# Kernel optimization log

Hardware: AMD Instinct MI355X
Metric: run time of the kernel (lower is better)

The kernel has to match this reference:

```python
import jax, jax.numpy as jnp
from jax import lax
import numpy as np

D_X, D_Y, HID = 64, 1, 128
D_NODES = D_X + 2          # d_x + 2
D_IN = D_X + 1 + D_Y       # fc_in input dim
K_LANGEVIN, ETA = 20, 0.01
BATCH = 8192


def setup_inputs() -> dict:
    key = jax.random.key(0)
    ks = jax.random.split(key, 12)
    s = 0.05
    return {
        "x": jax.random.normal(ks[0], (BATCH, D_X), jnp.float32),
        "t": jnp.ones((BATCH, 1), jnp.float32),
        "B_param": s * jax.random.normal(ks[1], (D_NODES, D_NODES), jnp.float32),
        "W_in": s * jax.random.normal(ks[2], (D_IN, HID), jnp.float32),
        "b_in": jnp.zeros((HID,), jnp.float32),
        "WT1": s * jax.random.normal(ks[3], (HID, HID), jnp.float32),
        "bT1": jnp.zeros((HID,), jnp.float32),
        "WT2": s * jax.random.normal(ks[4], (HID, 1), jnp.float32),
        "bT2": jnp.zeros((1,), jnp.float32),
        "WY1": s * jax.random.normal(ks[5], (HID, HID), jnp.float32),
        "bY1": jnp.zeros((HID,), jnp.float32),
        "WY2": s * jax.random.normal(ks[6], (HID, 1), jnp.float32),
        "bY2": jnp.zeros((1,), jnp.float32),
    }


def _mask():
    m = jnp.ones((D_NODES, D_NODES), jnp.float32)
    m = m.at[-1, :D_X].set(0.0)          # last node has no incoming edges from x-nodes
    m = m * (1.0 - jnp.eye(D_NODES, dtype=jnp.float32))  # zero diagonal
    return m


def _energy(z, x, B_param, mask, W_in, b_in, WT1, bT1, WT2, bT2, WY1, bY1, WY2, bY2):
    # z = [t, y] : [B, 1 + d_y]
    A = jax.nn.sigmoid(B_param) * mask                       # [N, N]
    h0 = jnp.concatenate([x, z], axis=-1) @ W_in + b_in      # [B, H]
    h = jnp.broadcast_to(h0[:, None, :], (h0.shape[0], D_NODES, HID))  # repeat over nodes
    # MaskedGraphConv: h + (A @ h) / d_nodes, then ReLU (x2)
    h = jax.nn.relu(h + jnp.einsum('ij,bjd->bid', A, h) / D_NODES)
    h = jax.nn.relu(h + jnp.einsum('ij,bjd->bid', A, h) / D_NODES)
    eT = jax.nn.relu(h[:, -2] @ WT1 + bT1) @ WT2 + bT2       # [B, 1]
    eY = jax.nn.relu(h[:, -1] @ WY1 + bY1) @ WY2 + bY2       # [B, 1]
    return (eT + eY)[:, 0]                                   # [B]


def reference(x, t, B_param, W_in, b_in, WT1, bT1, WT2, bT2, WY1, bY1, WY2, bY2):
    mask = _mask()
    grad_E = jax.grad(lambda z: _energy(z, x, B_param, mask, W_in, b_in,
                                        WT1, bT1, WT2, bT2, WY1, bY1, WY2, bY2).sum())
    z0 = jnp.concatenate([t, jnp.zeros((x.shape[0], D_Y), x.dtype)], axis=-1)
    sqrt_eta = jnp.sqrt(jnp.float32(ETA))

    def step(z, k):
        g = grad_E(z)
        noise = jax.random.normal(k, z.shape, z.dtype)
        return z - 0.5 * ETA * g + sqrt_eta * noise, None

    keys = jax.random.split(jax.random.key(42), K_LANGEVIN)
    z_final, _ = lax.scan(step, z0, keys)
    return z_final[:, 1:]   # predicted y, [B, d_y]
```

## Files before the change

### kernel.cpp

```cpp
#include <hip/hip_runtime.h>
#include <stdint.h>

#define NBATCH 8192
#define HID    128
#define DXC    64
#define NN     66
#define NSTEP  20
#define MROWS  16
#define RSTR   136
#define DSTR   280

typedef __attribute__((ext_vector_type(8))) short short8;
typedef __attribute__((ext_vector_type(4))) float f32x4;

static __device__ __forceinline__ ushort f2bf(float f) {
  union { float f; uint32_t u; } v; v.f = f;
  uint32_t u = v.u;
  u += 0x7fffu + ((u >> 16) & 1u);
  return (ushort)(u >> 16);
}

__device__ __forceinline__ void tf2x32(uint32_t k1, uint32_t k2,
                                       uint32_t x0, uint32_t x1,
                                       uint32_t &o0, uint32_t &o1) {
  uint32_t k3 = k1 ^ k2 ^ 0x1BD11BDAu;
  x0 += k1; x1 += k2;
#define RND(r) do { x0 += x1; x1 = (x1 << (r)) | (x1 >> (32 - (r))); x1 ^= x0; } while (0)
  RND(13); RND(15); RND(26); RND(6);
  x0 += k2; x1 += k3 + 1u;
  RND(17); RND(29); RND(16); RND(24);
  x0 += k3; x1 += k1 + 2u;
  RND(13); RND(15); RND(26); RND(6);
  x0 += k1; x1 += k2 + 3u;
  RND(17); RND(29); RND(16); RND(24);
  x0 += k2; x1 += k3 + 4u;
  RND(13); RND(15); RND(26); RND(6);
  x0 += k3; x1 += k1 + 5u;
#undef RND
  o0 = x0; o1 = x1;
}

__device__ __forceinline__ float erfinv_f(float x) {
  float w = -log1pf(-x * x);
  float p1, p2;
  {
    float ww = w - 2.5f;
    float p = 2.81022636e-08f;
    p = fmaf(p, ww, 3.43273939e-07f);
    p = fmaf(p, ww, -3.5233877e-06f);
    p = fmaf(p, ww, -4.39150654e-06f);
    p = fmaf(p, ww, 0.00021858087f);
    p = fmaf(p, ww, -0.00125372503f);
    p = fmaf(p, ww, -0.00417768164f);
    p = fmaf(p, ww, 0.246640727f);
    p = fmaf(p, ww, 1.50140941f);
    p1 = p;
  }
  {
    float ww = sqrtf(w) - 3.0f;
    float p = -0.000200214257f;
    p = fmaf(p, ww, 0.000100950558f);
    p = fmaf(p, ww, 0.00134934322f);
    p = fmaf(p, ww, -0.00367342844f);
    p = fmaf(p, ww, 0.00573950773f);
    p = fmaf(p, ww, -0.0076224613f);
    p = fmaf(p, ww, 0.00943887047f);
    p = fmaf(p, ww, 1.00167406f);
    p = fmaf(p, ww, 2.83297682f);
    p2 = p;
  }
  float p = (w < 5.0f) ? p1 : p2;
  return p * x;
}

__device__ __forceinline__ float bits_to_normal(uint32_t bits) {
  float f = __uint_as_float((bits >> 9) | 0x3F800000u) - 1.0f;
  const float LO = -0.99999994f;
  float u = fmaxf(LO, fmaf(f, 2.0f, LO));
  return 1.41421356237f * erfinv_f(u);
}

__global__ __launch_bounds__(256, 2) void ebm_fused(
    const float* __restrict__ x, const float* __restrict__ t_in,
    const float* __restrict__ Bp,
    const float* __restrict__ W_in, const float* __restrict__ b_in,
    const float* __restrict__ WT1, const float* __restrict__ bT1,
    const float* __restrict__ WT2,
    const float* __restrict__ WY1, const float* __restrict__ bY1,
    const float* __restrict__ WY2,
    float* __restrict__ out) {

  __shared__ __align__(16) ushort rT[MROWS * RSTR];
  __shared__ __align__(16) ushort duL[MROWS * DSTR];
  __shared__ float xs[MROWS * DXC];
  __shared__ float zt[MROWS], zy[MROWS];
  __shared__ float gpart[4][MROWS][2];
  __shared__ uint32_t skeys[NSTEP][2];
  __shared__ float cb[NN];
  __shared__ float dsc[2];

  const int tid  = threadIdx.x;
  const int lane = tid & 63;
  const int wv   = tid >> 6;
  const int r16  = lane & 15;
  const int q    = lane >> 4;
  const int brow0 = blockIdx.x * MROWS;

  ((float4*)xs)[tid] = ((const float4*)(x + (size_t)brow0 * DXC))[tid];
  if (tid < MROWS) { zt[tid] = t_in[brow0 + tid]; zy[tid] = 0.f; }
  if (tid < NSTEP) {
    uint32_t o0, o1;
    tf2x32(0u, 42u, 0u, (uint32_t)tid, o0, o1);
    skeys[tid][0] = o0; skeys[tid][1] = o1;
  }
  if (tid < NN) {
    float rs = 0.f;
    for (int j = 0; j < NN; ++j) {
      if (j == tid) continue;
      if (tid == NN - 1 && j < DXC) continue;
      float v = Bp[tid * NN + j];
      rs += 1.f / (1.f + expf(-v));
    }
    cb[tid] = 1.f + rs / 66.f;
  }
  __syncthreads();
  if (tid < 2) {
    int i = 64 + tid;
    float s = 0.f;
    for (int j = 0; j < NN; ++j) {
      if (j == i) continue;
      if (i == NN - 1 && j < DXC) continue;
      float v = Bp[i * NN + j];
      s += (1.f / (1.f + expf(-v))) * cb[j];
    }
    dsc[tid] = cb[i] + s / 66.f;
  }
  __syncthreads();
  const float d64 = dsc[0], d65 = dsc[1];

  const int n0 = 32 * wv + r16, n1 = n0 + 16;
  const float bT1a = bT1[n0], bT1b = bT1[n1];
  const float bY1a = bY1[n0], bY1b = bY1[n1];
  const ushort wT2a = f2bf(WT2[n0]), wT2b = f2bf(WT2[n1]);
  const ushort wY2a = f2bf(WY2[n0]), wY2b = f2bf(WY2[n1]);
  const float wtA = W_in[64 * HID + n0], wtB = W_in[64 * HID + n1];
  const float wyA = W_in[65 * HID + n0], wyB = W_in[65 * HID + n1];
  const float2 wtk2 = ((const float2*)(W_in + 64 * HID))[lane];
  const float2 wyk2 = ((const float2*)(W_in + 65 * HID))[lane];

  short8 fT0[4], fT1[4], fY0[4], fY1[4];
  short8 hT0[4], hT1[4], hY0[4], hY1[4];
#pragma unroll
  for (int kt = 0; kt < 4; ++kt) {
    const int kb = kt * 32 + q * 8;
    short8 a0, a1, b0, b1;
#pragma unroll
    for (int j = 0; j < 8; ++j) {
      a0[j] = (short)f2bf(d64 * WT1[(kb + j) * HID + n0]);
      a1[j] = (short)f2bf(d64 * WT1[(kb + j) * HID + n1]);
      b0[j] = (short)f2bf(d65 * WY1[(kb + j) * HID + n0]);
      b1[j] = (short)f2bf(d65 * WY1[(kb + j) * HID + n1]);
    }
    fT0[kt] = a0; fT1[kt] = a1; fY0[kt] = b0; fY1[kt] = b1;
    const float* pT0 = WT1 + (size_t)n0 * HID + kb;
    const float* pT1 = WT1 + (size_t)n1 * HID + kb;
    const float* pY0 = WY1 + (size_t)n0 * HID + kb;
    const float* pY1 = WY1 + (size_t)n1 * HID + kb;
    short8 c0v, c1v, e0, e1;
#pragma unroll
    for (int j = 0; j < 8; ++j) {
      c0v[j] = (short)f2bf(d64 * pT0[j]);
      c1v[j] = (short)f2bf(d64 * pT1[j]);
      e0[j]  = (short)f2bf(d65 * pY0[j]);
      e1[j]  = (short)f2bf(d65 * pY1[j]);
    }
    hT0[kt] = c0v; hT1[kt] = c1v; hY0[kt] = e0; hY1[kt] = e1;
  }

  float h0x_[4][2];
  {
    float2 b2 = ((const float2*)b_in)[lane];
#pragma unroll
    for (int m = 0; m < 4; ++m) { h0x_[m][0] = b2.x; h0x_[m][1] = b2.y; }
    for (int cc = 0; cc < DXC; ++cc) {
      float2 w2 = ((const float2*)(W_in + cc * HID))[lane];
#pragma unroll
      for (int m = 0; m < 4; ++m) {
        float xv = xs[(wv * 4 + m) * DXC + cc];
        h0x_[m][0] = fmaf(xv, w2.x, h0x_[m][0]);
        h0x_[m][1] = fmaf(xv, w2.y, h0x_[m][1]);
      }
    }
  }
  __syncthreads();

  for (int s = 0; s < NSTEP; ++s) {
#pragma unroll
    for (int m = 0; m < 4; ++m) {
      int mg = wv * 4 + m;
      float ztv = zt[mg], zyv = zy[mg];
      float h0 = fmaf(zyv, wyk2.x, fmaf(ztv, wtk2.x, h0x_[m][0]));
      float h1 = fmaf(zyv, wyk2.y, fmaf(ztv, wtk2.y, h0x_[m][1]));
      ushort lo = f2bf(fmaxf(h0, 0.f));
      ushort hi = f2bf(fmaxf(h1, 0.f));
      ((uint32_t*)rT)[mg * (RSTR / 2) + lane] = (uint32_t)lo | ((uint32_t)hi << 16);
    }
    __syncthreads();

    {
      short8 ar[4];
#pragma unroll
      for (int kt = 0; kt < 4; ++kt)
        ar[kt] = *reinterpret_cast<const short8*>(&rT[r16 * RSTR + kt * 32 + q * 8]);

      f32x4 aT0 = {0.f, 0.f, 0.f, 0.f}, aT1 = aT0, aY0 = aT0, aY1 = aT0;
#pragma unroll
      for (int kt = 0; kt < 4; ++kt) {
        aT0 = __builtin_amdgcn_mfma_f32_16x16x32_bf16(ar[kt], fT0[kt], aT0, 0, 0, 0);
        aT1 = __builtin_amdgcn_mfma_f32_16x16x32_bf16(ar[kt], fT1[kt], aT1, 0, 0, 0);
        aY0 = __builtin_amdgcn_mfma_f32_16x16x32_bf16(ar[kt], fY0[kt], aY0, 0, 0, 0);
        aY1 = __builtin_amdgcn_mfma_f32_16x16x32_bf16(ar[kt], fY1[kt], aY1, 0, 0, 0);
      }
#pragma unroll
      for (int reg = 0; reg < 4; ++reg) {
        int row = q * 4 + reg;
        duL[row * DSTR + n0]       = (aT0[reg] + bT1a > 0.f) ? wT2a : (ushort)0;
        duL[row * DSTR + n1]       = (aT1[reg] + bT1b > 0.f) ? wT2b : (ushort)0;
        duL[row * DSTR + 128 + n0] = (aY0[reg] + bY1a > 0.f) ? wY2a : (ushort)0;
        duL[row * DSTR + 128 + n1] = (aY1[reg] + bY1b > 0.f) ? wY2b : (ushort)0;
      }
    }
    __syncthreads();

    {
      short8 d8[4];
#pragma unroll
      for (int kt = 0; kt < 4; ++kt)
        d8[kt] = *reinterpret_cast<const short8*>(&duL[r16 * DSTR + kt * 32 + q * 8]);
      f32x4 g0 = {0.f, 0.f, 0.f, 0.f}, g1 = g0;
#pragma unroll
      for (int kt = 0; kt < 4; ++kt) {
        g0 = __builtin_amdgcn_mfma_f32_16x16x32_bf16(d8[kt], hT0[kt], g0, 0, 0, 0);
        g1 = __builtin_amdgcn_mfma_f32_16x16x32_bf16(d8[kt], hT1[kt], g1, 0, 0, 0);
      }
#pragma unroll
      for (int kt = 0; kt < 4; ++kt)
        d8[kt] = *reinterpret_cast<const short8*>(&duL[r16 * DSTR + 128 + kt * 32 + q * 8]);
#pragma unroll
      for (int kt = 0; kt < 4; ++kt) {
        g0 = __builtin_amdgcn_mfma_f32_16x16x32_bf16(d8[kt], hY0[kt], g0, 0, 0, 0);
        g1 = __builtin_amdgcn_mfma_f32_16x16x32_bf16(d8[kt], hY1[kt], g1, 0, 0, 0);
      }
      float pt[4], py[4];
#pragma unroll
      for (int reg = 0; reg < 4; ++reg) {
        int row = q * 4 + reg;
        short rv0 = (short)rT[row * RSTR + n0];
        short rv1 = (short)rT[row * RSTR + n1];
        float v0 = (rv0 > 0) ? g0[reg] : 0.f;
        float v1 = (rv1 > 0) ? g1[reg] : 0.f;
        pt[reg] = fmaf(v0, wtA, v1 * wtB);
        py[reg] = fmaf(v0, wyA, v1 * wyB);
      }
#pragma unroll
      for (int reg = 0; reg < 4; ++reg) {
#pragma unroll
        for (int off = 1; off < 16; off <<= 1) {
          pt[reg] += __shfl_xor(pt[reg], off);
          py[reg] += __shfl_xor(py[reg], off);
        }
      }
      if (r16 == 0) {
#pragma unroll
        for (int reg = 0; reg < 4; ++reg) {
          gpart[wv][q * 4 + reg][0] = pt[reg];
          gpart[wv][q * 4 + reg][1] = py[reg];
        }
      }
    }
    __syncthreads();

    if (tid < MROWS) {
      float gt = gpart[0][tid][0] + gpart[1][tid][0] + gpart[2][tid][0] + gpart[3][tid][0];
      float gy = gpart[0][tid][1] + gpart[1][tid][1] + gpart[2][tid][1] + gpart[3][tid][1];
      uint32_t idx = (uint32_t)(2 * (brow0 + tid));
      uint32_t o0, o1;
      tf2x32(skeys[s][0], skeys[s][1], 0u, idx, o0, o1);
      float nt = bits_to_normal(o0 ^ o1);
      tf2x32(skeys[s][0], skeys[s][1], 0u, idx + 1u, o0, o1);
      float ny = bits_to_normal(o0 ^ o1);
      zt[tid] = (zt[tid] - 0.005f * gt) + 0.1f * nt;
      zy[tid] = (zy[tid] - 0.005f * gy) + 0.1f * ny;
    }
    __syncthreads();
  }

  if (tid < MROWS) out[brow0 + tid] = zy[tid];
}

extern "C" void kernel_launch(void* const* d_in, const int* in_sizes, int n_in,
                              void* d_out, int out_size, void* d_ws, size_t ws_size,
                              hipStream_t stream) {
  const float* x    = (const float*)d_in[0];
  const float* t_in = (const float*)d_in[1];
  const float* Bp   = (const float*)d_in[2];
  const float* W_in = (const float*)d_in[3];
  const float* b_in = (const float*)d_in[4];
  const float* WT1  = (const float*)d_in[5];
  const float* bT1  = (const float*)d_in[6];
  const float* WT2  = (const float*)d_in[7];
  const float* WY1  = (const float*)d_in[9];
  const float* bY1  = (const float*)d_in[10];
  const float* WY2  = (const float*)d_in[11];
  float* out = (float*)d_out;

  ebm_fused<<<NBATCH / MROWS, 256, 0, stream>>>(
      x, t_in, Bp, W_in, b_in, WT1, bT1, WT2, WY1, bY1, WY2, out);
}
```

Baseline: 189.0 us.

## Use 512-thread blocks, precompute Langevin noise, keep z state in registers

Each block now runs eight waves instead of four, with every wave owning 16 hidden columns rather than 32. This halves the per-wave MFMA chain and the register-resident weight fragments. All 20 steps' Gaussian noise is generated up front into shared memory, which takes the Threefry/erfinv work off the serial per-step tail. The z state is held redundantly in registers by each row's thread group, removing one barrier and the single-thread update phase per step. The costs are more waves contending per CU and an eight-way partial-gradient reduction.

```diff
diff --git a/kernel.cpp b/kernel.cpp
--- a/kernel.cpp
+++ b/kernel.cpp
@@ -80,7 +80,7 @@
   return 1.41421356237f * erfinv_f(u);
 }
 
-__global__ __launch_bounds__(256, 2) void ebm_fused(
+__global__ __launch_bounds__(512, 4) void ebm_fused(
     const float* __restrict__ x, const float* __restrict__ t_in,
     const float* __restrict__ Bp,
     const float* __restrict__ W_in, const float* __restrict__ b_in,
@@ -92,9 +92,9 @@
 
   __shared__ __align__(16) ushort rT[MROWS * RSTR];
   __shared__ __align__(16) ushort duL[MROWS * DSTR];
-  __shared__ float xs[MROWS * DXC];
-  __shared__ float zt[MROWS], zy[MROWS];
-  __shared__ float gpart[4][MROWS][2];
+  __shared__ __align__(16) float xs[MROWS * DXC];
+  __shared__ float nbuf[NSTEP * 2 * MROWS];
+  __shared__ float gpart[8][MROWS][2];
   __shared__ uint32_t skeys[NSTEP][2];
   __shared__ float cb[NN];
   __shared__ float dsc[2];
@@ -104,10 +104,11 @@
   const int wv   = tid >> 6;
   const int r16  = lane & 15;
   const int q    = lane >> 4;
+  const int row  = tid >> 5;
+  const int c4   = (tid & 31) * 4;
   const int brow0 = blockIdx.x * MROWS;
 
-  ((float4*)xs)[tid] = ((const float4*)(x + (size_t)brow0 * DXC))[tid];
-  if (tid < MROWS) { zt[tid] = t_in[brow0 + tid]; zy[tid] = 0.f; }
+  if (tid < 256) ((float4*)xs)[tid] = ((const float4*)(x + (size_t)brow0 * DXC))[tid];
   if (tid < NSTEP) {
     uint32_t o0, o1;
     tf2x32(0u, 42u, 0u, (uint32_t)tid, o0, o1);
@@ -138,72 +139,78 @@
   __syncthreads();
   const float d64 = dsc[0], d65 = dsc[1];
 
-  const int n0 = 32 * wv + r16, n1 = n0 + 16;
-  const float bT1a = bT1[n0], bT1b = bT1[n1];
-  const float bY1a = bY1[n0], bY1b = bY1[n1];
-  const ushort wT2a = f2bf(WT2[n0]), wT2b = f2bf(WT2[n1]);
-  const ushort wY2a = f2bf(WY2[n0]), wY2b = f2bf(WY2[n1]);
-  const float wtA = W_in[64 * HID + n0], wtB = W_in[64 * HID + n1];
-  const float wyA = W_in[65 * HID + n0], wyB = W_in[65 * HID + n1];
-  const float2 wtk2 = ((const float2*)(W_in + 64 * HID))[lane];
-  const float2 wyk2 = ((const float2*)(W_in + 65 * HID))[lane];
-
-  short8 fT0[4], fT1[4], fY0[4], fY1[4];
-  short8 hT0[4], hT1[4], hY0[4], hY1[4];
+  for (int f = tid; f < NSTEP * 2 * MROWS; f += 512) {
+    int s = f >> 5, rr = f & 31;
+    uint32_t idx = (uint32_t)(2 * (brow0 + (rr >> 1)) + (rr & 1));
+    uint32_t o0, o1;
+    tf2x32(skeys[s][0], skeys[s][1], 0u, idx, o0, o1);
+    nbuf[f] = bits_to_normal(o0 ^ o1);
+  }
+
+  const int n0 = 16 * wv + r16;
+  const float bT1a = bT1[n0], bY1a = bY1[n0];
+  const ushort wT2a = f2bf(WT2[n0]), wY2a = f2bf(WY2[n0]);
+  const float wtA = W_in[64 * HID + n0], wyA = W_in[65 * HID + n0];
+  const float4 wtk4 = *(const float4*)(W_in + 64 * HID + c4);
+  const float4 wyk4 = *(const float4*)(W_in + 65 * HID + c4);
+
+  short8 fT[4], fY[4], hT[4], hY[4];
 #pragma unroll
   for (int kt = 0; kt < 4; ++kt) {
     const int kb = kt * 32 + q * 8;
-    short8 a0, a1, b0, b1;
+    short8 a, b;
 #pragma unroll
     for (int j = 0; j < 8; ++j) {
-      a0[j] = (short)f2bf(d64 * WT1[(kb + j) * HID + n0]);
-      a1[j] = (short)f2bf(d64 * WT1[(kb + j) * HID + n1]);
-      b0[j] = (short)f2bf(d65 * WY1[(kb + j) * HID + n0]);
-      b1[j] = (short)f2bf(d65 * WY1[(kb + j) * HID + n1]);
-    }
-    fT0[kt] = a0; fT1[kt] = a1; fY0[kt] = b0; fY1[kt] = b1;
-    const float* pT0 = WT1 + (size_t)n0 * HID + kb;
-    const float* pT1 = WT1 + (size_t)n1 * HID + kb;
-    const float* pY0 = WY1 + (size_t)n0 * HID + kb;
-    const float* pY1 = WY1 + (size_t)n1 * HID + kb;
-    short8 c0v, c1v, e0, e1;
-#pragma unroll
-    for (int j = 0; j < 8; ++j) {
-      c0v[j] = (short)f2bf(d64 * pT0[j]);
-      c1v[j] = (short)f2bf(d64 * pT1[j]);
-      e0[j]  = (short)f2bf(d65 * pY0[j]);
-      e1[j]  = (short)f2bf(d65 * pY1[j]);
-    }
-    hT0[kt] = c0v; hT1[kt] = c1v; hY0[kt] = e0; hY1[kt] = e1;
-  }
-
-  float h0x_[4][2];
+      a[j] = (short)f2bf(d64 * WT1[(kb + j) * HID + n0]);
+      b[j] = (short)f2bf(d65 * WY1[(kb + j) * HID + n0]);
+    }
+    fT[kt] = a; fY[kt] = b;
+    const float4* pT = (const float4*)(WT1 + (size_t)n0 * HID + kb);
+    const float4* pY = (const float4*)(WY1 + (size_t)n0 * HID + kb);
+    float4 t0 = pT[0], t1 = pT[1], y0 = pY[0], y1 = pY[1];
+    short8 c, e;
+    c[0] = (short)f2bf(d64 * t0.x); c[1] = (short)f2bf(d64 * t0.y);
+    c[2] = (short)f2bf(d64 * t0.z); c[3] = (short)f2bf(d64 * t0.w);
+    c[4] = (short)f2bf(d64 * t1.x); c[5] = (short)f2bf(d64 * t1.y);
+    c[6] = (short)f2bf(d64 * t1.z); c[7] = (short)f2bf(d64 * t1.w);
+    e[0] = (short)f2bf(d65 * y0.x); e[1] = (short)f2bf(d65 * y0.y);
+    e[2] = (short)f2bf(d65 * y0.z); e[3] = (short)f2bf(d65 * y0.w);
+    e[4] = (short)f2bf(d65 * y1.x); e[5] = (short)f2bf(d65 * y1.y);
+    e[6] = (short)f2bf(d65 * y1.z); e[7] = (short)f2bf(d65 * y1.w);
+    hT[kt] = c; hY[kt] = e;
+  }
+
+  float h0x_[4];
   {
-    float2 b2 = ((const float2*)b_in)[lane];
-#pragma unroll
-    for (int m = 0; m < 4; ++m) { h0x_[m][0] = b2.x; h0x_[m][1] = b2.y; }
+    float4 b4 = *(const float4*)(b_in + c4);
+    h0x_[0] = b4.x; h0x_[1] = b4.y; h0x_[2] = b4.z; h0x_[3] = b4.w;
     for (int cc = 0; cc < DXC; ++cc) {
-      float2 w2 = ((const float2*)(W_in + cc * HID))[lane];
-#pragma unroll
-      for (int m = 0; m < 4; ++m) {
-        float xv = xs[(wv * 4 + m) * DXC + cc];
-        h0x_[m][0] = fmaf(xv, w2.x, h0x_[m][0]);
-        h0x_[m][1] = fmaf(xv, w2.y, h0x_[m][1]);
-      }
-    }
-  }
+      float4 w4 = *(const float4*)(W_in + cc * HID + c4);
+      float xv = xs[row * DXC + cc];
+      h0x_[0] = fmaf(xv, w4.x, h0x_[0]);
+      h0x_[1] = fmaf(xv, w4.y, h0x_[1]);
+      h0x_[2] = fmaf(xv, w4.z, h0x_[2]);
+      h0x_[3] = fmaf(xv, w4.w, h0x_[3]);
+    }
+  }
+
+  float zt_r = t_in[brow0 + row];
+  float zy_r = 0.f;
   __syncthreads();
 
   for (int s = 0; s < NSTEP; ++s) {
-#pragma unroll
-    for (int m = 0; m < 4; ++m) {
-      int mg = wv * 4 + m;
-      float ztv = zt[mg], zyv = zy[mg];
-      float h0 = fmaf(zyv, wyk2.x, fmaf(ztv, wtk2.x, h0x_[m][0]));
-      float h1 = fmaf(zyv, wyk2.y, fmaf(ztv, wtk2.y, h0x_[m][1]));
-      ushort lo = f2bf(fmaxf(h0, 0.f));
-      ushort hi = f2bf(fmaxf(h1, 0.f));
-      ((uint32_t*)rT)[mg * (RSTR / 2) + lane] = (uint32_t)lo | ((uint32_t)hi << 16);
+    {
+      uint32_t p0, p1;
+      {
+        float h0 = fmaf(zy_r, wyk4.x, fmaf(zt_r, wtk4.x, h0x_[0]));
+        float h1 = fmaf(zy_r, wyk4.y, fmaf(zt_r, wtk4.y, h0x_[1]));
+        float h2 = fmaf(zy_r, wyk4.z, fmaf(zt_r, wtk4.z, h0x_[2]));
+        float h3 = fmaf(zy_r, wyk4.w, fmaf(zt_r, wtk4.w, h0x_[3]));
+        p0 = (uint32_t)f2bf(fmaxf(h0, 0.f)) | ((uint32_t)f2bf(fmaxf(h1, 0.f)) << 16);
+        p1 = (uint32_t)f2bf(fmaxf(h2, 0.f)) | ((uint32_t)f2bf(fmaxf(h3, 0.f)) << 16);
+      }
+      uint2 st; st.x = p0; st.y = p1;
+      *(uint2*)&rT[row * RSTR + c4] = st;
     }
     __syncthreads();
 
@@ -213,21 +220,17 @@
       for (int kt = 0; kt < 4; ++kt)
         ar[kt] = *reinterpret_cast<const short8*>(&rT[r16 * RSTR + kt * 32 + q * 8]);
 
-      f32x4 aT0 = {0.f, 0.f, 0.f, 0.f}, aT1 = aT0, aY0 = aT0, aY1 = aT0;
+      f32x4 aT = {0.f, 0.f, 0.f, 0.f}, aY = aT;
 #pragma unroll
       for (int kt = 0; kt < 4; ++kt) {
-        aT0 = __builtin_amdgcn_mfma_f32_16x16x32_bf16(ar[kt], fT0[kt], aT0, 0, 0, 0);
-        aT1 = __builtin_amdgcn_mfma_f32_16x16x32_bf16(ar[kt], fT1[kt], aT1, 0, 0, 0);
-        aY0 = __builtin_amdgcn_mfma_f32_16x16x32_bf16(ar[kt], fY0[kt], aY0, 0, 0, 0);
-        aY1 = __builtin_amdgcn_mfma_f32_16x16x32_bf16(ar[kt], fY1[kt], aY1, 0, 0, 0);
+        aT = __builtin_amdgcn_mfma_f32_16x16x32_bf16(ar[kt], fT[kt], aT, 0, 0, 0);
+        aY = __builtin_amdgcn_mfma_f32_16x16x32_bf16(ar[kt], fY[kt], aY, 0, 0, 0);
       }
 #pragma unroll
       for (int reg = 0; reg < 4; ++reg) {
-        int row = q * 4 + reg;
-        duL[row * DSTR + n0]       = (aT0[reg] + bT1a > 0.f) ? wT2a : (ushort)0;
-        duL[row * DSTR + n1]       = (aT1[reg] + bT1b > 0.f) ? wT2b : (ushort)0;
-        duL[row * DSTR + 128 + n0] = (aY0[reg] + bY1a > 0.f) ? wY2a : (ushort)0;
-        duL[row * DSTR + 128 + n1] = (aY1[reg] + bY1b > 0.f) ? wY2b : (ushort)0;
+        int rr = q * 4 + reg;
+        duL[rr * DSTR + n0]       = (aT[reg] + bT1a > 0.f) ? wT2a : (ushort)0;
+        duL[rr * DSTR + 128 + n0] = (aY[reg] + bY1a > 0.f) ? wY2a : (ushort)0;
       }
     }
     __syncthreads();
@@ -237,30 +240,25 @@
 #pragma unroll
       for (int kt = 0; kt < 4; ++kt)
         d8[kt] = *reinterpret_cast<const short8*>(&duL[r16 * DSTR + kt * 32 + q * 8]);
-      f32x4 g0 = {0.f, 0.f, 0.f, 0.f}, g1 = g0;
-#pragma unroll
-      for (int kt = 0; kt < 4; ++kt) {
-        g0 = __builtin_amdgcn_mfma_f32_16x16x32_bf16(d8[kt], hT0[kt], g0, 0, 0, 0);
-        g1 = __builtin_amdgcn_mfma_f32_16x16x32_bf16(d8[kt], hT1[kt], g1, 0, 0, 0);
-      }
+      f32x4 g = {0.f, 0.f, 0.f, 0.f};
+#pragma unroll
+      for (int kt = 0; kt < 4; ++kt)
+        g = __builtin_amdgcn_mfma_f32_16x16x32_bf16(d8[kt], hT[kt], g, 0, 0, 0);
 #pragma unroll
       for (int kt = 0; kt < 4; ++kt)
         d8[kt] = *reinterpret_cast<const short8*>(&duL[r16 * DSTR + 128 + kt * 32 + q * 8]);
 #pragma unroll
-      for (int kt = 0; kt < 4; ++kt) {
-        g0 = __builtin_amdgcn_mfma_f32_16x16x32_bf16(d8[kt], hY0[kt], g0, 0, 0, 0);
-        g1 = __builtin_amdgcn_mfma_f32_16x16x32_bf16(d8[kt], hY1[kt], g1, 0, 0, 0);
-      }
+      for (int kt = 0; kt < 4; ++kt)
+        g = __builtin_amdgcn_mfma_f32_16x16x32_bf16(d8[kt], hY[kt], g, 0, 0, 0);
+
       float pt[4], py[4];
 #pragma unroll
       for (int reg = 0; reg < 4; ++reg) {
-        int row = q * 4 + reg;
-        short rv0 = (short)rT[row * RSTR + n0];
-        short rv1 = (short)rT[row * RSTR + n1];
-        float v0 = (rv0 > 0) ? g0[reg] : 0.f;
-        float v1 = (rv1 > 0) ? g1[reg] : 0.f;
-        pt[reg] = fmaf(v0, wtA, v1 * wtB);
-        py[reg] = fmaf(v0, wyA, v1 * wyB);
+        int rr = q * 4 + reg;
+        short rv = (short)rT[rr * RSTR + n0];
+        float v = (rv > 0) ? g[reg] : 0.f;
+        pt[reg] = v * wtA;
+        py[reg] = v * wyA;
       }
 #pragma unroll
       for (int reg = 0; reg < 4; ++reg) {
@@ -280,22 +278,21 @@
     }
     __syncthreads();
 
-    if (tid < MROWS) {
-      float gt = gpart[0][tid][0] + gpart[1][tid][0] + gpart[2][tid][0] + gpart[3][tid][0];
-      float gy = gpart[0][tid][1] + gpart[1][tid][1] + gpart[2][tid][1] + gpart[3][tid][1];
-      uint32_t idx = (uint32_t)(2 * (brow0 + tid));
-      uint32_t o0, o1;
-      tf2x32(skeys[s][0], skeys[s][1], 0u, idx, o0, o1);
-      float nt = bits_to_normal(o0 ^ o1);
-      tf2x32(skeys[s][0], skeys[s][1], 0u, idx + 1u, o0, o1);
-      float ny = bits_to_normal(o0 ^ o1);
-      zt[tid] = (zt[tid] - 0.005f * gt) + 0.1f * nt;
-      zy[tid] = (zy[tid] - 0.005f * gy) + 0.1f * ny;
-    }
-    __syncthreads();
-  }
-
-  if (tid < MROWS) out[brow0 + tid] = zy[tid];
+    {
+      float gt = 0.f, gy = 0.f;
+#pragma unroll
+      for (int w = 0; w < 8; ++w) {
+        gt += gpart[w][row][0];
+        gy += gpart[w][row][1];
+      }
+      float nt = nbuf[s * 32 + 2 * row];
+      float ny = nbuf[s * 32 + 2 * row + 1];
+      zt_r = (zt_r - 0.005f * gt) + 0.1f * nt;
+      zy_r = (zy_r - 0.005f * gy) + 0.1f * ny;
+    }
+  }
+
+  if ((tid & 31) == 0) out[brow0 + row] = zy_r;
 }
 
 extern "C" void kernel_launch(void* const* d_in, const int* in_sizes, int n_in,
@@ -314,6 +311,6 @@
   const float* WY2  = (const float*)d_in[11];
   float* out = (float*)d_out;
 
-  ebm_fused<<<NBATCH / MROWS, 256, 0, stream>>>(
+  ebm_fused<<<NBATCH / MROWS, 512, 0, stream>>>(
       x, t_in, Bp, W_in, b_in, WT1, bT1, WT2, WY1, bY1, WY2, out);
 }
```

Result: no change. 185.8 us (-1.7%).
